# Performance work log

Measured on AMD Instinct MI355X. Metric: run time of the kernel, lower is better.

## Reference

```python
import jax, jax.numpy as jnp
import numpy as np
import math

B, SES, SEQ, H, K = 16, 16, 64, 512, 32
L = SES * SEQ


def setup_inputs() -> dict:
    key = jax.random.key(0)
    ks = jax.random.split(key, 16)
    s = 1.0 / math.sqrt(H)
    return {
        "user_emb": jax.random.normal(ks[0], (B, H), jnp.float32),
        "item_emb": jax.random.normal(ks[1], (B, SES, SEQ, H), jnp.float32),
        "mask": jnp.zeros((B, L, K), jnp.float32),
        "index": jax.random.randint(ks[2], (L, K), 0, L, jnp.int64),
        "Wq": jax.random.normal(ks[3], (H, H), jnp.float32) * s,
        "bq": jnp.zeros((H,), jnp.float32),
        "Wk": jax.random.normal(ks[4], (H, H), jnp.float32) * s,
        "bk": jnp.zeros((H,), jnp.float32),
        "Wv": jax.random.normal(ks[5], (H, H), jnp.float32) * s,
        "bv": jnp.zeros((H,), jnp.float32),
        "Wd": jax.random.normal(ks[6], (H, H), jnp.float32) * s,
        "bd": jnp.zeros((H,), jnp.float32),
        "ln_g": jnp.ones((H,), jnp.float32),
        "ln_b": jnp.zeros((H,), jnp.float32),
    }


def reference(user_emb, item_emb, mask, index, Wq, bq, Wk, bk, Wv, bv, Wd, bd, ln_g, ln_b):
    b, ses, seq, h = item_emb.shape
    l = ses * seq
    item_flat = item_emb.reshape(b, l, h)
    q = user_emb @ Wq.T + bq                       # [B, H]
    k = item_flat @ Wk.T + bk                      # [B, L, H]
    v = item_flat @ Wv.T + bv                      # [B, L, H]
    # scalar query against all L keys, scaled by sqrt(hidden_size)
    scores = jnp.einsum("bh,blh->bl", q, k) / math.sqrt(h)
    scores = scores[:, index] + mask               # gather -> [B, L, K]
    w = jax.nn.softmax(scores, axis=-1)            # [B, L, K]
    vg = v[:, index, :]                            # gather -> [B, L, K, H]
    attn_out = jnp.einsum("blk,blkh->blh", w, vg)  # [B, L, H]
    dense = attn_out @ Wd.T + bd
    x = dense + item_flat                          # residual (dropout = identity, eval)
    mu = jnp.mean(x, axis=-1, keepdims=True)
    var = jnp.var(x, axis=-1, keepdims=True)
    y = (x - mu) / jnp.sqrt(var + 1e-12) * ln_g + ln_b
    return y.reshape(b, ses, seq, h)
```

## Files before the change

kernel.cpp:

```cpp
#include <hip/hip_runtime.h>
#include <math.h>

constexpr int HD   = 512;
constexpr int LL   = 1024;
constexpr int MT   = 16384;
constexpr int KNBR = 32;
constexpr float SCL = 0.04419417382415922f;

typedef __attribute__((ext_vector_type(8))) short  bf16x8;
typedef __attribute__((ext_vector_type(4))) float  f32x4;

__device__ inline float b2f(unsigned short u) {
    union { unsigned int i; float f; } v; v.i = (unsigned int)u << 16; return v.f;
}
__device__ inline float b2f_lo(unsigned int u) {
    union { unsigned int i; float f; } v; v.i = u << 16; return v.f;
}
__device__ inline float b2f_hi(unsigned int u) {
    union { unsigned int i; float f; } v; v.i = u & 0xffff0000u; return v.f;
}
__device__ inline unsigned short f2b(float x) {
    union { float f; unsigned int u; } v; v.f = x;
    unsigned int r = v.u + 0x7fff + ((v.u >> 16) & 1);
    return (unsigned short)(r >> 16);
}

constexpr int PB_CONV_I = 8192;
constexpr int PB_CONV_W = 512;
constexpr int PB_Q      = 2048;

__global__ __launch_bounds__(256) void prep(
    const float* __restrict__ item, const float* __restrict__ Wv,
    const float* __restrict__ Wd, const float* __restrict__ u,
    const float* __restrict__ Wq, const float* __restrict__ bq,
    unsigned short* __restrict__ item_bf, unsigned short* __restrict__ item_kt,
    unsigned short* __restrict__ Wv_bf, unsigned short* __restrict__ Wd_bf,
    float* __restrict__ q)
{
    const int blk = blockIdx.x, tid = threadIdx.x;

    if (blk < PB_CONV_I) {
        const int i = blk * 1024 + tid * 4;
        float4 v = *(const float4*)&item[i];
        ushort4 o;
        o.x = f2b(v.x); o.y = f2b(v.y); o.z = f2b(v.z); o.w = f2b(v.w);
        *(ushort4*)&item_bf[i] = o;
        const int m = i >> 9, k = i & 511;
        *(ushort4*)&item_kt[((size_t)(k >> 5) * MT + m) * 32 + (k & 31)] = o;
        return;
    }
    if (blk < PB_CONV_I + PB_CONV_W) {
        const int n = HD*HD;
        const int i = (blk - PB_CONV_I) * 1024 + tid * 4;
        const float* s; unsigned short* d; int off;
        if (i < n) { s = Wv; d = Wv_bf; off = i; }
        else       { s = Wd; d = Wd_bf; off = i - n; }
        float4 v = *(const float4*)&s[off];
        ushort4 o;
        o.x = f2b(v.x); o.y = f2b(v.y); o.z = f2b(v.z); o.w = f2b(v.w);
        const int nr = off >> 9, k = off & 511;
        *(ushort4*)&d[((k >> 5) * 512 + nr) * 32 + (k & 31)] = o;
        return;
    }
    {
        const int wid  = (blk - PB_CONV_I - PB_CONV_W) * 4 + (tid >> 6);
        const int lane = tid & 63;
        const int b = wid >> 9, h = wid & 511;
        const float* ur = &u[b*HD + lane*8];
        const float* wr = &Wq[(size_t)h*HD + lane*8];
        const float4 u0 = *(const float4*)ur, u1 = *(const float4*)(ur+4);
        const float4 w0 = *(const float4*)wr, w1 = *(const float4*)(wr+4);
        float acc = u0.x*w0.x + u0.y*w0.y + u0.z*w0.z + u0.w*w0.w
                  + u1.x*w1.x + u1.y*w1.y + u1.z*w1.z + u1.w*w1.w;
        #pragma unroll
        for (int off = 32; off; off >>= 1) acc += __shfl_down(acc, off);
        if (lane == 0) q[b*HD + h] = acc + bq[h];
    }
}

__global__ __launch_bounds__(256) void gemm_v_r(
    const unsigned short* __restrict__ Akt, const unsigned short* __restrict__ Wt,
    const float* __restrict__ bv, const float* __restrict__ Wk,
    const float* __restrict__ bk, const float* __restrict__ q,
    unsigned short* __restrict__ v_bf, float* __restrict__ rbuf,
    float* __restrict__ s0buf)
{
    __shared__ unsigned short As[4][128 * 32];
    __shared__ unsigned short Bs[4][128 * 32];

    const int blk = blockIdx.x;
    const int tid = threadIdx.x;

    if (blk >= 512) {
        if (blk < 640) {
            __shared__ float red[4][64];
            const int rblk = blk - 512;
            const int b = rblk >> 3, c0 = (rblk & 7) * 64;
            const int cl = tid & 63, hg = tid >> 6;
            const float* qb = &q[b*HD];
            const float* wb = &Wk[(size_t)hg*128*HD + c0 + cl];
            float acc = 0.f;
            #pragma unroll 8
            for (int h = 0; h < 128; h++)
                acc += qb[hg*128 + h] * wb[(size_t)h*HD];
            red[hg][cl] = acc;
            __syncthreads();
            if (tid < 64)
                rbuf[b*HD + c0 + tid] = SCL *
                    (red[0][tid] + red[1][tid] + red[2][tid] + red[3][tid]);
        } else {
            __shared__ float sp[4];
            const int b = blk - 640;
            float p = q[b*HD + tid]*bk[tid] + q[b*HD + tid + 256]*bk[tid + 256];
            #pragma unroll
            for (int off = 32; off; off >>= 1) p += __shfl_down(p, off);
            if ((tid & 63) == 0) sp[tid >> 6] = p;
            __syncthreads();
            if (tid == 0) s0buf[b] = (sp[0] + sp[1] + sp[2] + sp[3]) * SCL;
        }
        return;
    }

    const int rowb = (blk & 7) | ((blk >> 5) << 3);
    const int colb = (blk >> 3) & 3;
    const int row0 = rowb * 128;
    const int col0 = colb * 128;

    const int wave = tid >> 6, lane = tid & 63;
    const int wm = (wave >> 1) * 64;
    const int wn = (wave & 1)  * 64;

    const int lrr = lane >> 2;
    const int cc  = lane & 3;
    int st_row[2], st_gchunk[2];
    #pragma unroll
    for (int t = 0; t < 2; t++) {
        const int m = wave*32 + t*16 + lrr;
        st_row[t]    = m;
        st_gchunk[t] = cc ^ ((m >> 1) & 3);
    }

    const int fr   = lane & 15;
    const int quad = lane >> 4;

    f32x4 acc[4][4];
    #pragma unroll
    for (int i = 0; i < 4; i++)
        #pragma unroll
        for (int j = 0; j < 4; j++)
            acc[i][j] = (f32x4){0.f, 0.f, 0.f, 0.f};

    int a_off[4], b_off[4];
    #pragma unroll
    for (int i = 0; i < 4; i++) {
        const int m = wm + i*16 + fr;
        a_off[i] = m*32 + ((quad ^ ((m >> 1) & 3)) << 3);
        const int n = wn + i*16 + fr;
        b_off[i] = n*32 + ((quad ^ ((n >> 1) & 3)) << 3);
    }

    auto stage = [&](int kt) {
        const int bf = kt & 3;
        #pragma unroll
        for (int t = 0; t < 2; t++) {
            const int m = st_row[t];
            const unsigned short* ga =
                &Akt[((size_t)kt*MT + row0 + m)*32 + st_gchunk[t]*8];
            __builtin_amdgcn_global_load_lds(
                (const __attribute__((address_space(1))) void*)ga,
                (__attribute__((address_space(3))) void*)&As[bf][(wave*32 + t*16)*32],
                16, 0, 0);
            const unsigned short* gw =
                &Wt[((size_t)kt*512 + col0 + m)*32 + st_gchunk[t]*8];
            __builtin_amdgcn_global_load_lds(
                (const __attribute__((address_space(1))) void*)gw,
                (__attribute__((address_space(3))) void*)&Bs[bf][(wave*32 + t*16)*32],
                16, 0, 0);
        }
    };

    auto kstep = [&](int cur, int kt_next) {
        __builtin_amdgcn_s_barrier();
        asm volatile("" ::: "memory");
        bf16x8 af[4], bfr[4];
        #pragma unroll
        for (int i = 0; i < 4; i++) {
            af[i]  = *(const bf16x8*)&As[cur][a_off[i]];
            bfr[i] = *(const bf16x8*)&Bs[cur][b_off[i]];
        }
        asm volatile("s_waitcnt lgkmcnt(0)" ::: "memory");
        __builtin_amdgcn_sched_barrier(0);
        __builtin_amdgcn_s_barrier();
        if (kt_next >= 0) stage(kt_next);
        __builtin_amdgcn_s_setprio(1);
        #pragma unroll
        for (int i = 0; i < 4; i++)
            #pragma unroll
            for (int j = 0; j < 4; j++)
                acc[i][j] = __builtin_amdgcn_mfma_f32_16x16x32_bf16(
                    af[i], bfr[j], acc[i][j], 0, 0, 0);
        __builtin_amdgcn_s_setprio(0);
    };

    stage(0); stage(1); stage(2); stage(3);

    for (int s = 0; s <= 12; ++s) {
        asm volatile("s_waitcnt vmcnt(12)" ::: "memory");
        kstep(s & 3, (s + 4 <= 15) ? s + 4 : -1);
    }
    asm volatile("s_waitcnt vmcnt(8)" ::: "memory");  kstep(1, -1);
    asm volatile("s_waitcnt vmcnt(4)" ::: "memory");  kstep(2, -1);
    asm volatile("s_waitcnt vmcnt(0)" ::: "memory");  kstep(3, -1);

    #pragma unroll
    for (int j = 0; j < 4; j++) {
        const int col = col0 + wn + j*16 + fr;
        const float bb = bv[col];
        #pragma unroll
        for (int i = 0; i < 4; i++) {
            #pragma unroll
            for (int r = 0; r < 4; r++) {
                const int row = row0 + wm + i*16 + quad*4 + r;
                v_bf[(size_t)row*HD + col] = f2b(acc[i][j][r] + bb);
            }
        }
    }
}

__global__ __launch_bounds__(256) void gp_scores(
    const float* __restrict__ rbuf, const float* __restrict__ s0buf,
    const unsigned short* __restrict__ item_bf, float* __restrict__ scores)
{
    const int m = blockIdx.x * 4 + (threadIdx.x >> 6);
    const int lane = threadIdx.x & 63;
    const int b = m >> 10;
    const unsigned short* ir = &item_bf[(size_t)m*HD + lane*8];
    const uint4 iv = *(const uint4*)ir;
    const float* rr = &rbuf[b*HD + lane*8];
    const float4 r0 = *(const float4*)rr;
    const float4 r1 = *(const float4*)(rr + 4);
    float acc = r0.x*b2f_lo(iv.x) + r0.y*b2f_hi(iv.x)
              + r0.z*b2f_lo(iv.y) + r0.w*b2f_hi(iv.y)
              + r1.x*b2f_lo(iv.z) + r1.y*b2f_hi(iv.z)
              + r1.z*b2f_lo(iv.w) + r1.w*b2f_hi(iv.w);
    #pragma unroll
    for (int off = 32; off; off >>= 1) acc += __shfl_down(acc, off);
    if (lane == 0) scores[m] = acc + s0buf[b];
}

__global__ __launch_bounds__(512) void dense_attn_ln(
    const float* __restrict__ scores, const int* __restrict__ index,
    const float* __restrict__ mask, const unsigned short* __restrict__ v,
    const unsigned short* __restrict__ Wt,
    const float* __restrict__ bd, const unsigned short* __restrict__ res,
    const float* __restrict__ ln_g, const float* __restrict__ ln_b,
    float* __restrict__ out)
{
    __shared__ unsigned short Bs[2][512 * 32];
    __shared__ unsigned short att[64 * 520];
    __shared__ float rsum[8][64], rsq[8][64];

    const int tid  = threadIdx.x;
    const int wave = tid >> 6, lane = tid & 63;
    const int bid  = blockIdx.x;
    const int rblk = (bid & 7) * 32 + (bid >> 3);
    const int row0 = rblk * 64;
    const int b    = row0 >> 10;

    const int lrr = lane >> 2, cc = lane & 3;

    auto stageW = [&](int bf, int kt) {
        #pragma unroll
        for (int t = 0; t < 4; t++) {
            const int n   = wave*64 + t*16 + lrr;
            const int gch = cc ^ ((n >> 1) & 3);
            const unsigned short* gw = &Wt[((size_t)kt*512 + n)*32 + gch*8];
            __builtin_amdgcn_global_load_lds(
                (const __attribute__((address_space(1))) void*)gw,
                (__attribute__((address_space(3))) void*)&Bs[bf][(wave*64 + t*16)*32],
                16, 0, 0);
        }
    };

    stageW(0, 0);
    stageW(1, 1);

    {
        const unsigned short* vb = v + (size_t)b * LL * HD;
        const int loff = lane * 8;
        const int t = lane & 31;
        for (int rr = 0; rr < 8; ++rr) {
            const int lrow = wave * 8 + rr;
            const int m = row0 + lrow;
            const int l = m & 1023;

            const int idx = index[l*KNBR + t];
            const float s = scores[b*LL + idx] + mask[(size_t)m*KNBR + t];

            float mx = s;
            #pragma unroll
            for (int off = 16; off; off >>= 1) mx = fmaxf(mx, __shfl_xor(mx, off));
            const float e = __expf(s - mx);
            float sum = e;
            #pragma unroll
            for (int off = 16; off; off >>= 1) sum += __shfl_xor(sum, off);
            const float w = e / sum;

            float a[8] = {};
            #pragma unroll 8
            for (int t2 = 0; t2 < KNBR; t2++) {
                const int   it = __builtin_amdgcn_readlane(idx, t2);
                const float wt = __int_as_float(
                    __builtin_amdgcn_readlane(__float_as_int(w), t2));
                const uint4 pv = *(const uint4*)(vb + (size_t)it*HD + loff);
                a[0] += wt * b2f_lo(pv.x); a[1] += wt * b2f_hi(pv.x);
                a[2] += wt * b2f_lo(pv.y); a[3] += wt * b2f_hi(pv.y);
                a[4] += wt * b2f_lo(pv.z); a[5] += wt * b2f_hi(pv.z);
                a[6] += wt * b2f_lo(pv.w); a[7] += wt * b2f_hi(pv.w);
            }
            uint4 o;
            o.x = (unsigned int)f2b(a[0]) | ((unsigned int)f2b(a[1]) << 16);
            o.y = (unsigned int)f2b(a[2]) | ((unsigned int)f2b(a[3]) << 16);
            o.z = (unsigned int)f2b(a[4]) | ((unsigned int)f2b(a[5]) << 16);
            o.w = (unsigned int)f2b(a[6]) | ((unsigned int)f2b(a[7]) << 16);
            const int byteoff = lrow*1040 + ((lane*16) ^ ((lrow & 7) << 4));
            *(uint4*)((char*)att + byteoff) = o;
        }
    }
    asm volatile("s_waitcnt lgkmcnt(0)" ::: "memory");
    __builtin_amdgcn_s_barrier();
    asm volatile("" ::: "memory");

    const int fr = lane & 15, quad = lane >> 4;
    const int wr = wave >> 2, wc = wave & 3;

    f32x4 acc[2][8];
    #pragma unroll
    for (int i = 0; i < 2; i++)
        #pragma unroll
        for (int j = 0; j < 8; j++)
            acc[i][j] = (f32x4){0.f, 0.f, 0.f, 0.f};

    int b_off[8];
    #pragma unroll
    for (int j = 0; j < 8; j++) {
        const int n = wc*128 + j*16 + fr;
        b_off[j] = n*32 + ((quad ^ ((n >> 1) & 3)) << 3);
    }
    int a_row[2];
    #pragma unroll
    for (int i = 0; i < 2; i++) a_row[i] = wr*32 + i*16 + fr;

    auto kstep = [&](int s, int kt_next) {
        __builtin_amdgcn_s_barrier();
        asm volatile("" ::: "memory");
        bf16x8 af[2], bfr[8];
        #pragma unroll
        for (int i = 0; i < 2; i++) {
            const int cb = (s*64 + quad*16) ^ ((a_row[i] & 7) << 4);
            af[i] = *(const bf16x8*)((const char*)att + a_row[i]*1040 + cb);
        }
        #pragma unroll
        for (int j = 0; j < 8; j++) bfr[j] = *(const bf16x8*)&Bs[s & 1][b_off[j]];
        asm volatile("s_waitcnt lgkmcnt(0)" ::: "memory");
        __builtin_amdgcn_sched_barrier(0);
        __builtin_amdgcn_s_barrier();
        if (kt_next >= 0) stageW(s & 1, kt_next);
        __builtin_amdgcn_s_setprio(1);
        #pragma unroll
        for (int i = 0; i < 2; i++)
            #pragma unroll
            for (int j = 0; j < 8; j++)
                acc[i][j] = __builtin_amdgcn_mfma_f32_16x16x32_bf16(
                    af[i], bfr[j], acc[i][j], 0, 0, 0);
        __builtin_amdgcn_s_setprio(0);
    };

    for (int s = 0; s < 15; ++s) {
        asm volatile("s_waitcnt vmcnt(4)" ::: "memory");
        kstep(s, (s + 2 < 16) ? s + 2 : -1);
    }
    asm volatile("s_waitcnt vmcnt(0)" ::: "memory");
    kstep(15, -1);
    __syncthreads();

    unsigned short* rs = (unsigned short*)Bs;
    #pragma unroll
    for (int u2 = 0; u2 < 8; u2++) {
        const int id = tid*8 + u2;
        const int rr = id >> 6, c8 = id & 63;
        *(uint4*)&rs[rr*512 + c8*8] =
            *(const uint4*)&res[(size_t)(row0 + rr)*HD + c8*8];
    }
    __syncthreads();

    float bdv[8], gv[8], lbv[8];
    #pragma unroll
    for (int j = 0; j < 8; j++) {
        const int col = wc*128 + j*16 + fr;
        bdv[j] = bd[col]; gv[j] = ln_g[col]; lbv[j] = ln_b[col];
    }

    #pragma unroll
    for (int i = 0; i < 2; i++) {
        #pragma unroll
        for (int r = 0; r < 4; r++) {
            const int lrow = wr*32 + i*16 + quad*4 + r;
            float a1 = 0.f, a2 = 0.f;
            #pragma unroll
            for (int j = 0; j < 8; j++) {
                const int col = wc*128 + j*16 + fr;
                float val = acc[i][j][r] + bdv[j] + b2f(rs[lrow*512 + col]);
                acc[i][j][r] = val;
                a1 += val; a2 += val*val;
            }
            #pragma unroll
            for (int off = 1; off < 16; off <<= 1) {
                a1 += __shfl_xor(a1, off);
                a2 += __shfl_xor(a2, off);
            }
            if (fr == 0) { rsum[wave][lrow] = a1; rsq[wave][lrow] = a2; }
        }
    }
    __syncthreads();

    #pragma unroll
    for (int i = 0; i < 2; i++) {
        #pragma unroll
        for (int r = 0; r < 4; r++) {
            const int lrow = wr*32 + i*16 + quad*4 + r;
            const int wb0 = wr*4;
            const float tot  = rsum[wb0][lrow] + rsum[wb0+1][lrow]
                             + rsum[wb0+2][lrow] + rsum[wb0+3][lrow];
            const float tot2 = rsq[wb0][lrow]  + rsq[wb0+1][lrow]
                             + rsq[wb0+2][lrow]  + rsq[wb0+3][lrow];
            const float mu  = tot * (1.f/HD);
            const float var = tot2 * (1.f/HD) - mu*mu;
            const float inv = rsqrtf(var + 1e-12f);
            const size_t gr = (size_t)(row0 + lrow) * HD;
            #pragma unroll
            for (int j = 0; j < 8; j++) {
                const int col = wc*128 + j*16 + fr;
                out[gr + col] = (acc[i][j][r] - mu)*inv*gv[j] + lbv[j];
            }
        }
    }
}

extern "C" void kernel_launch(void* const* d_in, const int* in_sizes, int n_in,
                              void* d_out, int out_size, void* d_ws, size_t ws_size,
                              hipStream_t stream) {
    const float* user_emb = (const float*)d_in[0];
    const float* item_emb = (const float*)d_in[1];
    const float* mask     = (const float*)d_in[2];
    const int*   index    = (const int*)  d_in[3];
    const float* Wq = (const float*)d_in[4];  const float* bq = (const float*)d_in[5];
    const float* Wk = (const float*)d_in[6];  const float* bk = (const float*)d_in[7];
    const float* Wv = (const float*)d_in[8];  const float* bv = (const float*)d_in[9];
    const float* Wd = (const float*)d_in[10]; const float* bd = (const float*)d_in[11];
    const float* ln_g = (const float*)d_in[12];
    const float* ln_b = (const float*)d_in[13];

    float* out = (float*)d_out;

    char* p = (char*)d_ws;
    unsigned short* item_bf = (unsigned short*)p; p += (size_t)MT*HD*2;
    unsigned short* item_kt = (unsigned short*)p; p += (size_t)MT*HD*2;
    unsigned short* v_bf    = (unsigned short*)p; p += (size_t)MT*HD*2;
    unsigned short* Wv_bf   = (unsigned short*)p; p += (size_t)HD*HD*2;
    unsigned short* Wd_bf   = (unsigned short*)p; p += (size_t)HD*HD*2;
    float* q      = (float*)p; p += 16*HD*4;
    float* rbuf   = (float*)p; p += 16*HD*4;
    float* s0buf  = (float*)p; p += 16*4;
    float* scores = (float*)p; p += MT*4;

    prep<<<PB_CONV_I + PB_CONV_W + PB_Q, 256, 0, stream>>>(
        item_emb, Wv, Wd, user_emb, Wq, bq,
        item_bf, item_kt, Wv_bf, Wd_bf, q);

    gemm_v_r<<<656, 256, 0, stream>>>(item_kt, Wv_bf, bv, Wk, bk, q,
                                      v_bf, rbuf, s0buf);

    gp_scores<<<MT/4, 256, 0, stream>>>(rbuf, s0buf, item_bf, scores);

    dense_attn_ln<<<256, 512, 0, stream>>>(scores, index, mask, v_bf,
                                           Wd_bf, bd, item_bf,
                                           ln_g, ln_b, out);
}
```

Measured before the change: 190.5 us.

## Halve dense_attn_ln row tile and stream Wd straight into registers

The fused attention/dense/LayerNorm kernel now runs 512 blocks of 256 threads, each handling 32 rows instead of 64. Each wave owns a 128-column slice across all rows. The Wd tiles are prefetched two k-steps ahead into register double buffers, replacing the global_load_lds LDS staging and its per-step barriers. This is meant to raise occupancy and fill the CUs better, and to remove LDS traffic and synchronisation in the GEMM loop. In exchange, every block rereads the whole weight matrix, doubling weight traffic from L2, and register pressure goes up.

New measurement: 190.9 us. No clear change (+0.2%).

```diff
diff --git a/kernel.cpp b/kernel.cpp
--- a/kernel.cpp
+++ b/kernel.cpp
@@ -248,7 +248,7 @@
     if (lane == 0) scores[m] = acc + s0buf[b];
 }
 
-__global__ __launch_bounds__(512) void dense_attn_ln(
+__global__ __launch_bounds__(256) void dense_attn_ln(
     const float* __restrict__ scores, const int* __restrict__ index,
     const float* __restrict__ mask, const unsigned short* __restrict__ v,
     const unsigned short* __restrict__ Wt,
@@ -256,34 +256,28 @@
     const float* __restrict__ ln_g, const float* __restrict__ ln_b,
     float* __restrict__ out)
 {
-    __shared__ unsigned short Bs[2][512 * 32];
-    __shared__ unsigned short att[64 * 520];
-    __shared__ float rsum[8][64], rsq[8][64];
+    __shared__ unsigned short att[32 * 528];
+    __shared__ float rsum[4][32], rsq[4][32];
 
     const int tid  = threadIdx.x;
     const int wave = tid >> 6, lane = tid & 63;
     const int bid  = blockIdx.x;
-    const int rblk = (bid & 7) * 32 + (bid >> 3);
-    const int row0 = rblk * 64;
+    const int rblk = (bid & 7) * 64 + (bid >> 3);
+    const int row0 = rblk * 32;
     const int b    = row0 >> 10;
 
-    const int lrr = lane >> 2, cc = lane & 3;
-
-    auto stageW = [&](int bf, int kt) {
-        #pragma unroll
-        for (int t = 0; t < 4; t++) {
-            const int n   = wave*64 + t*16 + lrr;
-            const int gch = cc ^ ((n >> 1) & 3);
-            const unsigned short* gw = &Wt[((size_t)kt*512 + n)*32 + gch*8];
-            __builtin_amdgcn_global_load_lds(
-                (const __attribute__((address_space(1))) void*)gw,
-                (__attribute__((address_space(3))) void*)&Bs[bf][(wave*64 + t*16)*32],
-                16, 0, 0);
-        }
+    const int fr = lane & 15, quad = lane >> 4;
+
+    const unsigned short* wbase = Wt + ((size_t)wave*128 + fr)*32 + quad*8;
+    auto loadW = [&](int kt, bf16x8* dst) {
+        #pragma unroll
+        for (int j = 0; j < 8; j++)
+            dst[j] = *(const bf16x8*)(wbase + (size_t)kt*512*32 + j*16*32);
     };
 
-    stageW(0, 0);
-    stageW(1, 1);
+    bf16x8 wreg[2][8];
+    loadW(0, wreg[0]);
+    loadW(1, wreg[1]);
 
     {
         const unsigned short* vb = v + (size_t)b * LL * HD;
@@ -327,12 +321,7 @@
             *(uint4*)((char*)att + byteoff) = o;
         }
     }
-    asm volatile("s_waitcnt lgkmcnt(0)" ::: "memory");
-    __builtin_amdgcn_s_barrier();
-    asm volatile("" ::: "memory");
-
-    const int fr = lane & 15, quad = lane >> 4;
-    const int wr = wave >> 2, wc = wave & 3;
+    __syncthreads();
 
     f32x4 acc[2][8];
     #pragma unroll
@@ -341,55 +330,37 @@
         for (int j = 0; j < 8; j++)
             acc[i][j] = (f32x4){0.f, 0.f, 0.f, 0.f};
 
-    int b_off[8];
-    #pragma unroll
-    for (int j = 0; j < 8; j++) {
-        const int n = wc*128 + j*16 + fr;
-        b_off[j] = n*32 + ((quad ^ ((n >> 1) & 3)) << 3);
-    }
     int a_row[2];
     #pragma unroll
-    for (int i = 0; i < 2; i++) a_row[i] = wr*32 + i*16 + fr;
-
-    auto kstep = [&](int s, int kt_next) {
-        __builtin_amdgcn_s_barrier();
-        asm volatile("" ::: "memory");
-        bf16x8 af[2], bfr[8];
+    for (int i = 0; i < 2; i++) a_row[i] = i*16 + fr;
+
+    #pragma unroll
+    for (int s = 0; s < 16; ++s) {
+        bf16x8 af[2];
         #pragma unroll
         for (int i = 0; i < 2; i++) {
             const int cb = (s*64 + quad*16) ^ ((a_row[i] & 7) << 4);
             af[i] = *(const bf16x8*)((const char*)att + a_row[i]*1040 + cb);
         }
-        #pragma unroll
-        for (int j = 0; j < 8; j++) bfr[j] = *(const bf16x8*)&Bs[s & 1][b_off[j]];
-        asm volatile("s_waitcnt lgkmcnt(0)" ::: "memory");
-        __builtin_amdgcn_sched_barrier(0);
-        __builtin_amdgcn_s_barrier();
-        if (kt_next >= 0) stageW(s & 1, kt_next);
-        __builtin_amdgcn_s_setprio(1);
+        bf16x8 cur[8];
+        #pragma unroll
+        for (int j = 0; j < 8; j++) cur[j] = wreg[s & 1][j];
         #pragma unroll
         for (int i = 0; i < 2; i++)
             #pragma unroll
             for (int j = 0; j < 8; j++)
                 acc[i][j] = __builtin_amdgcn_mfma_f32_16x16x32_bf16(
-                    af[i], bfr[j], acc[i][j], 0, 0, 0);
-        __builtin_amdgcn_s_setprio(0);
-    };
-
-    for (int s = 0; s < 15; ++s) {
-        asm volatile("s_waitcnt vmcnt(4)" ::: "memory");
-        kstep(s, (s + 2 < 16) ? s + 2 : -1);
-    }
-    asm volatile("s_waitcnt vmcnt(0)" ::: "memory");
-    kstep(15, -1);
+                    af[i], cur[j], acc[i][j], 0, 0, 0);
+        if (s + 2 < 16) loadW(s + 2, wreg[s & 1]);
+    }
     __syncthreads();
 
-    unsigned short* rs = (unsigned short*)Bs;
+    unsigned short* rs = att;
     #pragma unroll
     for (int u2 = 0; u2 < 8; u2++) {
         const int id = tid*8 + u2;
         const int rr = id >> 6, c8 = id & 63;
-        *(uint4*)&rs[rr*512 + c8*8] =
+        *(uint4*)&rs[rr*528 + c8*8] =
             *(const uint4*)&res[(size_t)(row0 + rr)*HD + c8*8];
     }
     __syncthreads();
@@ -397,7 +368,7 @@
     float bdv[8], gv[8], lbv[8];
     #pragma unroll
     for (int j = 0; j < 8; j++) {
-        const int col = wc*128 + j*16 + fr;
+        const int col = wave*128 + j*16 + fr;
         bdv[j] = bd[col]; gv[j] = ln_g[col]; lbv[j] = ln_b[col];
     }
 
@@ -405,12 +376,12 @@
     for (int i = 0; i < 2; i++) {
         #pragma unroll
         for (int r = 0; r < 4; r++) {
-            const int lrow = wr*32 + i*16 + quad*4 + r;
+            const int lrow = i*16 + quad*4 + r;
             float a1 = 0.f, a2 = 0.f;
             #pragma unroll
             for (int j = 0; j < 8; j++) {
-                const int col = wc*128 + j*16 + fr;
-                float val = acc[i][j][r] + bdv[j] + b2f(rs[lrow*512 + col]);
+                const int col = wave*128 + j*16 + fr;
+                float val = acc[i][j][r] + bdv[j] + b2f(rs[lrow*528 + col]);
                 acc[i][j][r] = val;
                 a1 += val; a2 += val*val;
             }
@@ -428,19 +399,18 @@
     for (int i = 0; i < 2; i++) {
         #pragma unroll
         for (int r = 0; r < 4; r++) {
-            const int lrow = wr*32 + i*16 + quad*4 + r;
-            const int wb0 = wr*4;
-            const float tot  = rsum[wb0][lrow] + rsum[wb0+1][lrow]
-                             + rsum[wb0+2][lrow] + rsum[wb0+3][lrow];
-            const float tot2 = rsq[wb0][lrow]  + rsq[wb0+1][lrow]
-                             + rsq[wb0+2][lrow]  + rsq[wb0+3][lrow];
+            const int lrow = i*16 + quad*4 + r;
+            const float tot  = rsum[0][lrow] + rsum[1][lrow]
+                             + rsum[2][lrow] + rsum[3][lrow];
+            const float tot2 = rsq[0][lrow]  + rsq[1][lrow]
+                             + rsq[2][lrow]  + rsq[3][lrow];
             const float mu  = tot * (1.f/HD);
             const float var = tot2 * (1.f/HD) - mu*mu;
             const float inv = rsqrtf(var + 1e-12f);
             const size_t gr = (size_t)(row0 + lrow) * HD;
             #pragma unroll
             for (int j = 0; j < 8; j++) {
-                const int col = wc*128 + j*16 + fr;
+                const int col = wave*128 + j*16 + fr;
                 out[gr + col] = (acc[i][j][r] - mu)*inv*gv[j] + lbv[j];
             }
         }
@@ -483,7 +453,7 @@
 
     gp_scores<<<MT/4, 256, 0, stream>>>(rbuf, s0buf, item_bf, scores);
 
-    dense_attn_ln<<<256, 512, 0, stream>>>(scores, index, mask, v_bf,
+    dense_attn_ln<<<512, 256, 0, stream>>>(scores, index, mask, v_bf,
                                            Wd_bf, bd, item_bf,
                                            ln_g, ln_b, out);
 }
```
